# Performance work log

Measured on AMD Instinct MI355X. Metric: run time of the kernel, lower is better.

The kernel has to match this reference:

```python
import jax, jax.numpy as jnp
import numpy as np

# ---- static configuration (from init_kwargs) ----
K = 2                 # kernel_size -> (2K+1)^2 = 25 window offsets
WIN = 2 * K + 1       # 5
A = WIN * WIN         # 25 window slots (ir_in replicated A times)
MUL_IN = 16           # multiplicity of each input irrep (16x0e + 16x1e)
MUL_OUT = 32          # 32x0e + 32x1e
SH0 = float(1.0 / (2.0 * np.sqrt(np.pi)))       # Y_l=0, e3nn 'integral' norm
SH1 = float(np.sqrt(3.0 / (4.0 * np.pi)))       # Y_l=1 scale (normalize=False)
CG_110 = float(1.0 / np.sqrt(3.0))              # CG for 1x1 -> 0 (dot/sqrt3)
CG_111 = float(1.0 / np.sqrt(2.0))              # CG for 1x1 -> 1 (cross/sqrt2)
# path normalization: out irrep gets 1/sqrt(fan_in) with fan = n_paths * mul_u
A0 = float(1.0 / np.sqrt(2 * A * MUL_IN))       # 0e fed by paths (0e,0e)+(1e,1e) per slot
A1 = float(1.0 / np.sqrt(3 * A * MUL_IN))       # 1e fed by (0e,1e)+(1e,0e)+(1e,1e)


def setup_inputs() -> dict:
    key = jax.random.key(0)
    ks = jax.random.split(key, 7)
    feat = jax.random.normal(ks[0], (8, 64, 64, 64), dtype=jnp.float32)
    spin = jax.random.normal(ks[1], (8, 64, 64, 3), dtype=jnp.float32)
    wshape = (A, MUL_IN, MUL_OUT)  # one uvw block per window slot per path type
    W_000 = jax.random.normal(ks[2], wshape, dtype=jnp.float32)
    W_110 = jax.random.normal(ks[3], wshape, dtype=jnp.float32)
    W_011 = jax.random.normal(ks[4], wshape, dtype=jnp.float32)
    W_101 = jax.random.normal(ks[5], wshape, dtype=jnp.float32)
    W_111 = jax.random.normal(ks[6], wshape, dtype=jnp.float32)
    return {"feat": feat, "spin": spin, "W_000": W_000, "W_110": W_110,
            "W_011": W_011, "W_101": W_101, "W_111": W_111}


def spin2colsq2d(feat):
    # circular im2col: (N,Lx,Ly,F) -> (N,Lx,Ly,A,F)
    N, Lx, Ly, F = feat.shape
    p = jnp.pad(feat, ((0, 0), (K, K), (K, K), (0, 0)), mode='wrap')
    cols = [p[:, ix:ix + Lx, iy:iy + Ly, :]
            for ix in range(WIN) for iy in range(WIN)]
    return jnp.stack(cols, axis=3)


def reference(feat, spin, W_000, W_110, W_011, W_101, W_111):
    col = spin2colsq2d(feat)                                  # (N,Lx,Ly,A,64)
    x0 = col[..., :MUL_IN]                                    # (N,Lx,Ly,A,16) scalars
    x1 = col[..., MUL_IN:].reshape(col.shape[:-1] + (MUL_IN, 3))  # (N,Lx,Ly,A,16,3)
    # spherical harmonics of spin, l=0..1, normalize=False, integral norm
    sh1 = SH1 * spin                                          # (N,Lx,Ly,3)
    # ---- paths into 0e output ----
    dot = jnp.einsum('nxyaui,nxyi->nxyau', x1, sh1) * CG_110  # 1e x 1e -> 0e
    out0 = A0 * (SH0 * jnp.einsum('nxyau,auw->nxyw', x0, W_000)
                 + jnp.einsum('nxyau,auw->nxyw', dot, W_110))  # (N,Lx,Ly,32)
    # ---- paths into 1e output ----
    cross = jnp.cross(x1, sh1[..., None, None, :]) * CG_111   # 1e x 1e -> 1e
    out1 = A1 * (jnp.einsum('nxyau,nxyi,auw->nxywi', x0, sh1, W_011)
                 + SH0 * jnp.einsum('nxyaui,auw->nxywi', x1, W_101)
                 + jnp.einsum('nxyaui,auw->nxywi', cross, W_111))  # (N,Lx,Ly,32,3)
    out1 = out1.reshape(out1.shape[:-2] + (MUL_OUT * 3,))
    return jnp.concatenate([out0, out1], axis=-1)             # (N,Lx,Ly,128)
```

## Files before the change

kernel.cpp:

```cpp
#include <hip/hip_runtime.h>


typedef __attribute__((ext_vector_type(8))) short short8;
typedef __attribute__((ext_vector_type(16))) float f32x16;
typedef __attribute__((ext_vector_type(4))) float float4v;

typedef __attribute__((address_space(3))) unsigned char lds_u8_t;
typedef const __attribute__((address_space(1))) unsigned char g_u8_t;

#define FEATT_BYTES (8u * 64u * 64u * 64u * 2u)
#define BT_OFFSET   FEATT_BYTES

#define MFMA32(A, B, C) __builtin_amdgcn_mfma_f32_32x32x16_bf16(A, B, C, 0, 0, 0)

__device__ __forceinline__ unsigned short f2bf(float f) {
    unsigned int u = __float_as_uint(f);
    return (unsigned short)((u + 0x7FFFu + ((u >> 16) & 1u)) >> 16);
}

__global__ __launch_bounds__(256) void prep_kernel(
    const float* __restrict__ feat,
    const float* __restrict__ W000, const float* __restrict__ W110,
    const float* __restrict__ W011, const float* __restrict__ W101,
    const float* __restrict__ W111,
    unsigned char* __restrict__ ws)
{
    int tid = threadIdx.x;
    int b = blockIdx.x;
    if (b < 512) {
        __shared__ float sf[64][68];
        size_t base = (size_t)b * 4096;
        #pragma unroll
        for (int i = 0; i < 4; ++i) {
            int e = tid + i * 256;
            float4v v = *(const float4v*)(feat + base + (size_t)e * 4);
            int px = e >> 4;
            int c  = (e & 15) * 4;
            sf[px][c + 0] = v[0]; sf[px][c + 1] = v[1];
            sf[px][c + 2] = v[2]; sf[px][c + 3] = v[3];
        }
        __syncthreads();
        unsigned short* dst = (unsigned short*)ws + base;
        #pragma unroll
        for (int i = 0; i < 2; ++i) {
            int t = tid + i * 256;
            int s = t >> 6, px = t & 63;
            short8 o;
            #pragma unroll
            for (int j = 0; j < 8; ++j) {
                int chp = s * 8 + j;
                int c = (chp < 16) ? chp : (16 + 3 * ((chp - 16) & 15) + ((chp - 16) >> 4));
                o[j] = (short)f2bf(sf[px][c]);
            }
            *(short8*)(dst + s * 512 + px * 8) = o;
        }
    } else {
        int t = (b - 512) * 256 + tid;
        if (t >= 4000) return;
        int a = t / 160, colv = t - a * 160;
        int arr = colv >> 5, w = colv & 31;
        const float* Wp = (arr == 0) ? W000 : (arr == 1) ? W011
                        : (arr == 2) ? W110 : (arr == 3) ? W101 : W111;
        unsigned short tmp[16];
        #pragma unroll
        for (int k = 0; k < 16; ++k) tmp[k] = f2bf(Wp[a * 512 + k * 32 + w]);
        unsigned short* d = (unsigned short*)(ws + BT_OFFSET) + (size_t)t * 16;
        *(short8*)(d)     = *(short8*)(tmp);
        *(short8*)(d + 8) = *(short8*)(tmp + 8);
    }
}

__global__ __launch_bounds__(512, 4) void spinconv_mfma_kernel(
    const unsigned char* __restrict__ featT8,
    const unsigned char* __restrict__ bt,
    const float* __restrict__ spin,
    float* __restrict__ out)
{
    const float SH0f   = 0.28209479177387814f;
    const float CG110f = 0.5773502691896258f;
    const float CG111f = 0.7071067811865476f;
    const float A0f    = 0.035355339059327376f;
    const float A1f    = 0.028867513459481287f;

    __shared__ __align__(16) unsigned char fl[5 * 8 * 64 * 16];
    __shared__ float s_lds[192];

    int tid = threadIdx.x;
    int b = blockIdx.x;
    int bid = ((b & 7) << 6) + (b >> 3);
    int x = bid & 63;

    int lane = tid & 63;
    int wv8 = tid >> 6;

    #pragma unroll
    for (int i = 0; i < 5; ++i) {
        int g = wv8 * 5 + i;
        int dx = g >> 3;
        int X = (x + dx + 62) & 63;
        const unsigned char* src = featT8
            + (size_t)(bid - x + X) * 8192 + (g & 7) * 1024 + lane * 16;
        __builtin_amdgcn_global_load_lds((g_u8_t*)src, (lds_u8_t*)(fl + g * 1024), 16, 0, 0);
    }
    if (tid < 192) {
        s_lds[tid] = 0.4886025119029199f * spin[(size_t)bid * 192 + tid];
    }
    __syncthreads();

    int pair = wv8 >> 2;
    int role = (wv8 + pair) & 3;
    int col = lane & 31;
    int khalf = lane >> 5;
    int yb = pair << 5;
    int p0 = bid << 6;

    const unsigned char* bbase = bt + col * 32 + khalf * 16;
    float* rowbuf = (float*)fl;

    f32x16 zz;
    #pragma unroll
    for (int i = 0; i < 16; ++i) zz[i] = 0.f;

    f32x16 ac0 = zz, ac1 = zz, ac2 = zz;

    if (role == 0) {
        short8 B0c, B1c, B0n, B1n, Axc, Axn;
        auto loadB = [&](int a, short8& b0, short8& b1) {
            const unsigned char* p = bbase + a * 5120;
            b0 = *(const short8*)(p);
            b1 = *(const short8*)(p + 1024);
        };
        auto loadA = [&](int a, short8& ax) {
            int ix = a / 5;
            int iy = a - ix * 5;
            int yn = (yb + col + iy + 62) & 63;
            ax = *(const short8*)(fl + ix * 8192 + yn * 16 + khalf * 1024);
        };
        loadB(0, B0c, B1c);
        loadA(0, Axc);
        #pragma unroll
        for (int ap = 0; ap < 25; ap += 2) {
            if (ap + 1 < 25) { loadB(ap + 1, B0n, B1n); loadA(ap + 1, Axn); }
            __builtin_amdgcn_s_setprio(1);
            ac0 = MFMA32(Axc, B0c, ac0);
            ac1 = MFMA32(Axc, B1c, ac1);
            __builtin_amdgcn_s_setprio(0);
            if (ap + 1 < 25) {
                if (ap + 2 < 25) { loadB(ap + 2, B0c, B1c); loadA(ap + 2, Axc); }
                __builtin_amdgcn_s_setprio(1);
                ac0 = MFMA32(Axn, B0n, ac0);
                ac1 = MFMA32(Axn, B1n, ac1);
                __builtin_amdgcn_s_setprio(0);
            }
        }
    } else {
        const int matoff = (role + 1) << 10;
        short8 Bc, Bn, C0c, C1c, C2c, C0n, C1n, C2n;
        auto loadB = [&](int a, short8& bb) {
            bb = *(const short8*)(bbase + a * 5120 + matoff);
        };
        auto loadA = [&](int a, short8& c0, short8& c1, short8& c2) {
            int ix = a / 5;
            int iy = a - ix * 5;
            int yn = (yb + col + iy + 62) & 63;
            const unsigned char* ab = fl + ix * 8192 + yn * 16;
            c0 = *(const short8*)(ab + (2 + khalf) * 1024);
            c1 = *(const short8*)(ab + (4 + khalf) * 1024);
            c2 = *(const short8*)(ab + (6 + khalf) * 1024);
        };
        loadB(0, Bc);
        loadA(0, C0c, C1c, C2c);
        #pragma unroll
        for (int ap = 0; ap < 25; ap += 2) {
            if (ap + 1 < 25) { loadB(ap + 1, Bn); loadA(ap + 1, C0n, C1n, C2n); }
            __builtin_amdgcn_s_setprio(1);
            ac0 = MFMA32(C0c, Bc, ac0);
            ac1 = MFMA32(C1c, Bc, ac1);
            ac2 = MFMA32(C2c, Bc, ac2);
            __builtin_amdgcn_s_setprio(0);
            if (ap + 1 < 25) {
                if (ap + 2 < 25) { loadB(ap + 2, Bc); loadA(ap + 2, C0c, C1c, C2c); }
                __builtin_amdgcn_s_setprio(1);
                ac0 = MFMA32(C0n, Bn, ac0);
                ac1 = MFMA32(C1n, Bn, ac1);
                ac2 = MFMA32(C2n, Bn, ac2);
                __builtin_amdgcn_s_setprio(0);
            }
        }
    }

    __syncthreads();

    #pragma unroll
    for (int ph = 0; ph < 4; ++ph) {
        if (role == ph) {
            #pragma unroll
            for (int r = 0; r < 16; ++r) {
                int row = (r & 3) + ((r >> 2) << 3) + (khalf << 2);
                int y = yb + row;
                float s0 = s_lds[y * 3 + 0];
                float s1 = s_lds[y * 3 + 1];
                float s2 = s_lds[y * 3 + 2];
                float* rb = rowbuf + y * 128;
                float* rp = rb + 32 + 3 * col;
                if (ph == 0) {
                    float S000 = ac0[r], S011 = ac1[r];
                    rb[col] = A0f * SH0f * S000;
                    rp[0] = A1f * s0 * S011;
                    rp[1] = A1f * s1 * S011;
                    rp[2] = A1f * s2 * S011;
                } else if (ph == 1) {
                    rb[col] += A0f * CG110f * (s0 * ac0[r] + s1 * ac1[r] + s2 * ac2[r]);
                } else if (ph == 2) {
                    rp[0] += A1f * SH0f * ac0[r];
                    rp[1] += A1f * SH0f * ac1[r];
                    rp[2] += A1f * SH0f * ac2[r];
                } else {
                    float U0 = ac0[r], U1 = ac1[r], U2 = ac2[r];
                    rp[0] += A1f * CG111f * (U1 * s2 - U2 * s1);
                    rp[1] += A1f * CG111f * (U2 * s0 - U0 * s2);
                    rp[2] += A1f * CG111f * (U0 * s1 - U1 * s0);
                }
            }
        }
        __syncthreads();
    }

    float* ob = out + (size_t)p0 * 128;
    #pragma unroll
    for (int i = 0; i < 4; ++i) {
        int e = (tid + (i << 9)) << 2;
        *(float4v*)(ob + e) = *(const float4v*)(rowbuf + e);
    }
}

extern "C" void kernel_launch(void* const* d_in, const int* in_sizes, int n_in,
                              void* d_out, int out_size, void* d_ws, size_t ws_size,
                              hipStream_t stream) {
    const float* feat = (const float*)d_in[0];
    const float* spin = (const float*)d_in[1];
    const float* W000 = (const float*)d_in[2];
    const float* W110 = (const float*)d_in[3];
    const float* W011 = (const float*)d_in[4];
    const float* W101 = (const float*)d_in[5];
    const float* W111 = (const float*)d_in[6];
    float* out = (float*)d_out;
    unsigned char* ws = (unsigned char*)d_ws;

    hipLaunchKernelGGL(prep_kernel, dim3(528), dim3(256), 0, stream,
                       feat, W000, W110, W011, W101, W111, ws);
    hipLaunchKernelGGL(spinconv_mfma_kernel, dim3(512), dim3(512), 0, stream,
                       ws, ws + BT_OFFSET, spin, out);
}
```

Measured before the change: 24.78 us.

## Split each column into half-column blocks of four waves with compact halo LDS

Each block now covers 32 y positions of one x column using 4 waves instead of 64 positions with 8 waves, doubling the grid to 1024 blocks. Only the needed 36-row y halo per dx and slot is staged in LDS (1440 16-byte entries), and the epilogue merges the role-1 and role-2 phases so there are three barriers instead of four. The intent is better occupancy and load balance with less LDS per block. In exchange, overlapping halos mean more redundant feature loads, and the LDS layout and indexing are more complex.

```diff
diff --git a/kernel.cpp b/kernel.cpp
--- a/kernel.cpp
+++ b/kernel.cpp
@@ -70,7 +70,7 @@
     }
 }
 
-__global__ __launch_bounds__(512, 4) void spinconv_mfma_kernel(
+__global__ __launch_bounds__(256, 4) void spinconv_mfma_kernel(
     const unsigned char* __restrict__ featT8,
     const unsigned char* __restrict__ bt,
     const float* __restrict__ spin,
@@ -82,37 +82,42 @@
     const float A0f    = 0.035355339059327376f;
     const float A1f    = 0.028867513459481287f;
 
-    __shared__ __align__(16) unsigned char fl[5 * 8 * 64 * 16];
-    __shared__ float s_lds[192];
+    __shared__ __align__(16) unsigned char fl[1440 * 16];
+    __shared__ float s_lds[96];
 
     int tid = threadIdx.x;
     int b = blockIdx.x;
-    int bid = ((b & 7) << 6) + (b >> 3);
-    int x = bid & 63;
+    int L = ((b & 7) << 7) + (b >> 3);
+    int column = L >> 1;
+    int x = column & 63;
+    int y0 = (L & 1) << 5;
 
     int lane = tid & 63;
-    int wv8 = tid >> 6;
+    int wv4 = tid >> 6;
 
     #pragma unroll
-    for (int i = 0; i < 5; ++i) {
-        int g = wv8 * 5 + i;
-        int dx = g >> 3;
+    for (int i = 0; i < 6; ++i) {
+        int e = tid + (i << 8);
+        int g = e / 36;
+        int l = e - g * 36;
+        int dx = g >> 3, slot = g & 7;
         int X = (x + dx + 62) & 63;
+        int y = (y0 + l + 62) & 63;
         const unsigned char* src = featT8
-            + (size_t)(bid - x + X) * 8192 + (g & 7) * 1024 + lane * 16;
-        __builtin_amdgcn_global_load_lds((g_u8_t*)src, (lds_u8_t*)(fl + g * 1024), 16, 0, 0);
-    }
-    if (tid < 192) {
-        s_lds[tid] = 0.4886025119029199f * spin[(size_t)bid * 192 + tid];
+            + (size_t)(column - x + X) * 8192 + slot * 1024 + y * 16;
+        if (e < 1440)
+            __builtin_amdgcn_global_load_lds((g_u8_t*)src,
+                (lds_u8_t*)(fl + ((i << 8) + (tid & ~63)) * 16), 16, 0, 0);
+    }
+    if (tid < 96) {
+        s_lds[tid] = 0.4886025119029199f
+                   * spin[((size_t)column * 64 + y0) * 3 + tid];
     }
     __syncthreads();
 
-    int pair = wv8 >> 2;
-    int role = (wv8 + pair) & 3;
+    int role = (wv4 + (b & 3)) & 3;
     int col = lane & 31;
     int khalf = lane >> 5;
-    int yb = pair << 5;
-    int p0 = bid << 6;
 
     const unsigned char* bbase = bt + col * 32 + khalf * 16;
     float* rowbuf = (float*)fl;
@@ -133,8 +138,7 @@
         auto loadA = [&](int a, short8& ax) {
             int ix = a / 5;
             int iy = a - ix * 5;
-            int yn = (yb + col + iy + 62) & 63;
-            ax = *(const short8*)(fl + ix * 8192 + yn * 16 + khalf * 1024);
+            ax = *(const short8*)(fl + ix * 4608 + khalf * 576 + (col + iy) * 16);
         };
         loadB(0, B0c, B1c);
         loadA(0, Axc);
@@ -162,11 +166,10 @@
         auto loadA = [&](int a, short8& c0, short8& c1, short8& c2) {
             int ix = a / 5;
             int iy = a - ix * 5;
-            int yn = (yb + col + iy + 62) & 63;
-            const unsigned char* ab = fl + ix * 8192 + yn * 16;
-            c0 = *(const short8*)(ab + (2 + khalf) * 1024);
-            c1 = *(const short8*)(ab + (4 + khalf) * 1024);
-            c2 = *(const short8*)(ab + (6 + khalf) * 1024);
+            const unsigned char* ab = fl + ix * 4608 + (col + iy) * 16;
+            c0 = *(const short8*)(ab + (2 + khalf) * 576);
+            c1 = *(const short8*)(ab + (4 + khalf) * 576);
+            c2 = *(const short8*)(ab + (6 + khalf) * 576);
         };
         loadB(0, Bc);
         loadA(0, C0c, C1c, C2c);
@@ -191,45 +194,66 @@
 
     __syncthreads();
 
-    #pragma unroll
-    for (int ph = 0; ph < 4; ++ph) {
-        if (role == ph) {
-            #pragma unroll
-            for (int r = 0; r < 16; ++r) {
-                int row = (r & 3) + ((r >> 2) << 3) + (khalf << 2);
-                int y = yb + row;
-                float s0 = s_lds[y * 3 + 0];
-                float s1 = s_lds[y * 3 + 1];
-                float s2 = s_lds[y * 3 + 2];
-                float* rb = rowbuf + y * 128;
+    {
+        if (role == 0) {
+            #pragma unroll
+            for (int r = 0; r < 16; ++r) {
+                int yl = (r & 3) + ((r >> 2) << 3) + (khalf << 2);
+                float s0 = s_lds[yl * 3 + 0];
+                float s1 = s_lds[yl * 3 + 1];
+                float s2 = s_lds[yl * 3 + 2];
+                float S000 = ac0[r], S011 = ac1[r];
+                float* rb = rowbuf + yl * 128;
                 float* rp = rb + 32 + 3 * col;
-                if (ph == 0) {
-                    float S000 = ac0[r], S011 = ac1[r];
-                    rb[col] = A0f * SH0f * S000;
-                    rp[0] = A1f * s0 * S011;
-                    rp[1] = A1f * s1 * S011;
-                    rp[2] = A1f * s2 * S011;
-                } else if (ph == 1) {
-                    rb[col] += A0f * CG110f * (s0 * ac0[r] + s1 * ac1[r] + s2 * ac2[r]);
-                } else if (ph == 2) {
-                    rp[0] += A1f * SH0f * ac0[r];
-                    rp[1] += A1f * SH0f * ac1[r];
-                    rp[2] += A1f * SH0f * ac2[r];
-                } else {
-                    float U0 = ac0[r], U1 = ac1[r], U2 = ac2[r];
-                    rp[0] += A1f * CG111f * (U1 * s2 - U2 * s1);
-                    rp[1] += A1f * CG111f * (U2 * s0 - U0 * s2);
-                    rp[2] += A1f * CG111f * (U0 * s1 - U1 * s0);
-                }
-            }
-        }
-        __syncthreads();
-    }
-
-    float* ob = out + (size_t)p0 * 128;
+                rb[col] = A0f * SH0f * S000;
+                rp[0] = A1f * s0 * S011;
+                rp[1] = A1f * s1 * S011;
+                rp[2] = A1f * s2 * S011;
+            }
+        }
+        __syncthreads();
+        if (role == 1) {
+            #pragma unroll
+            for (int r = 0; r < 16; ++r) {
+                int yl = (r & 3) + ((r >> 2) << 3) + (khalf << 2);
+                float s0 = s_lds[yl * 3 + 0];
+                float s1 = s_lds[yl * 3 + 1];
+                float s2 = s_lds[yl * 3 + 2];
+                rowbuf[yl * 128 + col] +=
+                    A0f * CG110f * (s0 * ac0[r] + s1 * ac1[r] + s2 * ac2[r]);
+            }
+        } else if (role == 2) {
+            #pragma unroll
+            for (int r = 0; r < 16; ++r) {
+                int yl = (r & 3) + ((r >> 2) << 3) + (khalf << 2);
+                float* rp = rowbuf + yl * 128 + 32 + 3 * col;
+                rp[0] += A1f * SH0f * ac0[r];
+                rp[1] += A1f * SH0f * ac1[r];
+                rp[2] += A1f * SH0f * ac2[r];
+            }
+        }
+        __syncthreads();
+        if (role == 3) {
+            #pragma unroll
+            for (int r = 0; r < 16; ++r) {
+                int yl = (r & 3) + ((r >> 2) << 3) + (khalf << 2);
+                float s0 = s_lds[yl * 3 + 0];
+                float s1 = s_lds[yl * 3 + 1];
+                float s2 = s_lds[yl * 3 + 2];
+                float U0 = ac0[r], U1 = ac1[r], U2 = ac2[r];
+                float* rp = rowbuf + yl * 128 + 32 + 3 * col;
+                rp[0] += A1f * CG111f * (U1 * s2 - U2 * s1);
+                rp[1] += A1f * CG111f * (U2 * s0 - U0 * s2);
+                rp[2] += A1f * CG111f * (U0 * s1 - U1 * s0);
+            }
+        }
+        __syncthreads();
+    }
+
+    float* ob = out + ((size_t)column * 64 + y0) * 128;
     #pragma unroll
     for (int i = 0; i < 4; ++i) {
-        int e = (tid + (i << 9)) << 2;
+        int e = (tid + (i << 8)) << 2;
         *(float4v*)(ob + e) = *(const float4v*)(rowbuf + e);
     }
 }
@@ -249,6 +273,6 @@
 
     hipLaunchKernelGGL(prep_kernel, dim3(528), dim3(256), 0, stream,
                        feat, W000, W110, W011, W101, W111, ws);
-    hipLaunchKernelGGL(spinconv_mfma_kernel, dim3(512), dim3(512), 0, stream,
+    hipLaunchKernelGGL(spinconv_mfma_kernel, dim3(1024), dim3(256), 0, stream,
                        ws, ws + BT_OFFSET, spin, out);
 }
```

Measured after the change: 24.60 us. About the same (-0.7%).
